# Optimization experiments

Hardware: AMD Instinct MI355X
Metric: run time of the kernel (lower is better)

Reference implementation:

```python
import jax, jax.numpy as jnp
import numpy as np

SLOPE = 25.0   # snntorch surrogate.fast_sigmoid default slope
THR = 1.0      # snntorch Leaky default threshold
BETA = 0.95
SPIKE_STEPS = 4
NUM_HEADS = 16

@jax.custom_vjp
def spike(u):
    # Heaviside forward, fast-sigmoid surrogate backward
    return (u > 0).astype(u.dtype)

def _spike_fwd(u):
    return spike(u), u

def _spike_bwd(u, g):
    return (g / (SLOPE * jnp.abs(u) + 1.0) ** 2,)

spike.defvjp(_spike_fwd, _spike_bwd)

def lif_mean(cur):
    """Run SPIKE_STEPS of a snntorch Leaky neuron (subtract reset, detached)
    with constant input current `cur`; return mean spike train over time."""
    def step(mem, _):
        reset = jax.lax.stop_gradient(spike(mem - THR))
        mem = BETA * mem + cur - reset * THR
        return mem, spike(mem - THR)
    _, spk = jax.lax.scan(step, jnp.zeros_like(cur), None, length=SPIKE_STEPS)
    return spk.mean(axis=0)

def setup_inputs() -> dict:
    B, S, D = 2, 2048, 1024
    key = jax.random.key(0)
    ks = jax.random.split(key, 9)
    std = 1.0 / np.sqrt(D)
    mkw = lambda k: jax.random.uniform(k, (D, D), jnp.float32, -std, std)
    mkb = lambda k: jax.random.uniform(k, (D,), jnp.float32, -std, std)
    return {
        "x": jax.random.normal(ks[0], (B, S, D), jnp.float32),
        "q_w": mkw(ks[1]), "q_b": mkb(ks[2]),
        "k_w": mkw(ks[3]), "k_b": mkb(ks[4]),
        "v_w": mkw(ks[5]), "v_b": mkb(ks[6]),
        "o_w": mkw(ks[7]), "o_b": mkb(ks[8]),
    }

def reference(x, q_w, q_b, k_w, k_b, v_w, v_b, o_w, o_b):
    B, S, D = x.shape
    H = NUM_HEADS
    Hd = D // H
    # projections -> [B, H, S, Hd]  (weights stored [in, out])
    proj = lambda w, b: (x @ w + b).reshape(B, S, H, Hd).transpose(0, 2, 1, 3)
    q, k, v = proj(q_w, q_b), proj(k_w, k_b), proj(v_w, v_b)
    # LIF spiking recurrence, aggregated over time
    q_agg, k_agg, v_agg = lif_mean(q), lif_mean(k), lif_mean(v)
    # standard scaled dot-product attention on aggregated spikes
    scores = jnp.einsum('bhqd,bhkd->bhqk', q_agg, k_agg) / jnp.sqrt(jnp.float32(Hd))
    attn = jax.nn.softmax(scores, axis=-1)
    out = jnp.einsum('bhqk,bhkd->bhqd', attn, v_agg)
    out = out.transpose(0, 2, 1, 3).reshape(B, S, D)
    return out @ o_w + o_b
```

## Files before the change

kernel.cpp:

```cpp
#include <hip/hip_runtime.h>
#include <hip/hip_bf16.h>
#include <stdint.h>

typedef unsigned short u16;
typedef unsigned int u32;
typedef __bf16 bf16x8 __attribute__((ext_vector_type(8)));
typedef float f32x4 __attribute__((ext_vector_type(4)));
typedef float f32x16 __attribute__((ext_vector_type(16)));
typedef u32 u32x4 __attribute__((ext_vector_type(4)));

#define B_   2
#define S_   2048
#define D_   1024
#define H_   16
#define HD_  64

__device__ __forceinline__ u16 f2bf(float f) {
    u32 u = __float_as_uint(f);
    u32 r = (u + 0x7FFFu + ((u >> 16) & 1u)) >> 16;
    return (u16)r;
}
__device__ __forceinline__ float bf2f(u16 s) { return __uint_as_float(((u32)s) << 16); }

__device__ __forceinline__ f32x4 mfma16(bf16x8 a, bf16x8 b, f32x4 c) {
    return __builtin_amdgcn_mfma_f32_16x16x32_bf16(a, b, c, 0, 0, 0);
}
__device__ __forceinline__ f32x16 mfma32(bf16x8 a, bf16x8 b, f32x16 c) {
    return __builtin_amdgcn_mfma_f32_32x32x16_bf16(a, b, c, 0, 0, 0);
}

__device__ __forceinline__ void gl16(const u16* g, u16* l) {
    __builtin_amdgcn_global_load_lds(
        (const __attribute__((address_space(1))) void*)g,
        (__attribute__((address_space(3))) void*)l, 16, 0, 0);
}

__global__ void prep_kernel(const float* __restrict__ x,
                            const float* __restrict__ qw, const float* __restrict__ kw,
                            const float* __restrict__ vw, const float* __restrict__ ow,
                            u16* __restrict__ xbf, u16* __restrict__ wt_all) {
    __shared__ float tile[32][33];
    const int bid = blockIdx.x;
    const int t = threadIdx.x;
    if (bid < 4096) {
        int i = bid * 256 + t;
        float4 v = reinterpret_cast<const float4*>(x)[i];
        uint2 hp;
        hp.x = (u32)f2bf(v.x) | ((u32)f2bf(v.y) << 16);
        hp.y = (u32)f2bf(v.z) | ((u32)f2bf(v.w) << 16);
        reinterpret_cast<uint2*>(xbf)[i] = hp;
        return;
    }
    const int f = bid - 4096;
    const int z = f >> 10;
    const int bi = (f & 1023) >> 5;
    const int bj = f & 31;
    const float* w = (z == 0) ? qw : (z == 1) ? kw : (z == 2) ? vw : ow;
    u16* thi = wt_all + (size_t)z * 1048576;
    const int tx = t & 31, ty = t >> 5;
#pragma unroll
    for (int k = 0; k < 4; k++) {
        int r = ty + k * 8;
        tile[r][tx] = w[(size_t)(bi * 32 + r) * D_ + bj * 32 + tx];
    }
    __syncthreads();
#pragma unroll
    for (int k = 0; k < 4; k++) {
        int r = ty + k * 8;
        thi[(size_t)(bj * 32 + r) * D_ + bi * 32 + tx] = f2bf(tile[tx][r]);
    }
}

__global__ __launch_bounds__(256, 3)
void qkv_gemm(const u16* __restrict__ Ag, const u16* __restrict__ Bg,
              const float* __restrict__ qb, const float* __restrict__ kb,
              const float* __restrict__ vb,
              u16* __restrict__ o0, u16* __restrict__ o1, u16* __restrict__ o2) {
    __shared__ __align__(16) u16 lA[3][128 * 32];
    __shared__ __align__(16) u16 lB[3][128 * 32];

    const int t = threadIdx.x;
    const int flat = blockIdx.y * 24 + blockIdx.x;
    const int swz = (flat & 7) * 96 + (flat >> 3);
    const int m0 = (swz / 24) * 128;
    const int n0 = (swz % 24) * 128;
    const int wid = t >> 6, lane = t & 63;
    const int wm = wid >> 1, wn = wid & 1;
    const int lr = lane & 15, lg = lane >> 4;

    f32x4 acc[4][4] = {};

    auto STAGE = [&](int buf, int kk) {
        const int k0 = kk * 32;
#pragma unroll
        for (int p = 0; p < 2; p++) {
            int idx = p * 256 + wid * 64 + lane;
            int row = idx >> 2, sl = idx & 3;
            int slx = sl ^ ((row >> 1) & 3);
            gl16(Ag + (size_t)(m0 + row) * D_ + k0 + slx * 8,
                 &lA[buf][(p * 256 + wid * 64) * 8]);
            gl16(Bg + (size_t)(n0 + row) * D_ + k0 + slx * 8,
                 &lB[buf][(p * 256 + wid * 64) * 8]);
        }
    };

    STAGE(0, 0);
    STAGE(1, 1);

    for (int kk = 0; kk < 32; ++kk) {
        if (kk < 31) asm volatile("s_waitcnt vmcnt(4)" ::: "memory");
        else         asm volatile("s_waitcnt vmcnt(0)" ::: "memory");
        __builtin_amdgcn_s_barrier();
        if (kk < 30) STAGE((kk + 2) % 3, kk + 2);

        const int cur = kk % 3;
        bf16x8 af[4], bf[4];
#pragma unroll
        for (int m = 0; m < 4; m++) {
            int row = wm * 64 + m * 16 + lr;
            af[m] = *reinterpret_cast<const bf16x8*>(
                &lA[cur][row * 32 + (lg ^ ((row >> 1) & 3)) * 8]);
        }
#pragma unroll
        for (int n = 0; n < 4; n++) {
            int row = wn * 64 + n * 16 + lr;
            bf[n] = *reinterpret_cast<const bf16x8*>(
                &lB[cur][row * 32 + (lg ^ ((row >> 1) & 3)) * 8]);
        }
#pragma unroll
        for (int m = 0; m < 4; m++)
#pragma unroll
            for (int n = 0; n < 4; n++)
                acc[m][n] = mfma16(af[m], bf[n], acc[m][n]);
    }

    const int col0f = n0 + wn * 64;
    const int proj = col0f >> 10;
    const float* bp = (proj == 0) ? qb : (proj == 1) ? kb : vb;
    u16* dst = (proj == 0) ? o0 : (proj == 1) ? o1 : o2;
#pragma unroll
    for (int m = 0; m < 4; m++) {
#pragma unroll
        for (int n = 0; n < 4; n++) {
            u16 agg4[4];
#pragma unroll
            for (int r = 0; r < 4; r++) {
                int row = m0 + wm * 64 + m * 16 + lg * 4 + r;
                int colp = (col0f + n * 16 + lr) & 1023;
                float cur_i = acc[m][n][r] + bp[colp];
                float mem = 0.f;
                int cnt = 0;
#pragma unroll
                for (int tt = 0; tt < 4; tt++) {
                    float reset = (mem > 1.f) ? 1.f : 0.f;
                    mem = 0.95f * mem;
                    mem = mem + cur_i;
                    mem = mem - reset;
                    cnt += (mem > 1.f) ? 1 : 0;
                }
                u16 agg = (u16)(__float_as_uint((float)cnt * 0.25f) >> 16);
                if (proj != 2) {
                    int b = row >> 11, s = row & 2047;
                    int h = colp >> 6, d = colp & 63;
                    dst[((size_t)(b * H_ + h) * S_ + s) * HD_ + d] = agg;
                } else {
                    agg4[r] = agg;
                }
            }
            if (proj == 2) {
                int row0 = m0 + wm * 64 + m * 16 + lg * 4;
                int colp = (col0f + n * 16 + lr) & 1023;
                int b = row0 >> 11, s = row0 & 2047;
                int h = colp >> 6, d = colp & 63;
                uint2 pk;
                pk.x = (u32)agg4[0] | ((u32)agg4[1] << 16);
                pk.y = (u32)agg4[2] | ((u32)agg4[3] << 16);
                *reinterpret_cast<uint2*>(
                    &dst[((size_t)(b * H_ + h) * HD_ + d) * S_ + s]) = pk;
            }
        }
    }
}

__global__ __launch_bounds__(256, 4)
void o_gemm(const u16* __restrict__ Ag, const u16* __restrict__ Bhg,
            const float* __restrict__ bias, float* __restrict__ out) {
    __shared__ __align__(16) u16 lA[3][64 * 32];
    __shared__ __align__(16) u16 lB[3][64 * 32];

    const int t = threadIdx.x;
    const int flat = blockIdx.y * 16 + blockIdx.x;
    const int swz = (flat & 7) * 128 + (flat >> 3);
    const int m0 = (swz >> 4) * 64;
    const int n0 = (swz & 15) * 64;
    const int wid = t >> 6, lane = t & 63;
    const int wm = wid >> 1, wn = wid & 1;
    const int lr = lane & 15, lg = lane >> 4;

    f32x4 acc[2][2] = {};

    auto STAGE = [&](int buf, int kk) {
        const int k0 = kk * 32;
        int idx = wid * 64 + lane;
        int row = idx >> 2, sl = idx & 3;
        int slx = sl ^ ((row >> 1) & 3);
        gl16(Ag + (size_t)(m0 + row) * D_ + k0 + slx * 8,
             &lA[buf][(wid * 64) * 8]);
        gl16(Bhg + (size_t)(n0 + row) * D_ + k0 + slx * 8,
             &lB[buf][(wid * 64) * 8]);
    };

    STAGE(0, 0);
    STAGE(1, 1);

    for (int kk = 0; kk < 32; ++kk) {
        if (kk < 31) asm volatile("s_waitcnt vmcnt(2)" ::: "memory");
        else         asm volatile("s_waitcnt vmcnt(0)" ::: "memory");
        __builtin_amdgcn_s_barrier();
        if (kk < 30) STAGE((kk + 2) % 3, kk + 2);

        const int cur = kk % 3;
        bf16x8 af[2], bf[2];
#pragma unroll
        for (int m = 0; m < 2; m++) {
            int row = wm * 32 + m * 16 + lr;
            af[m] = *reinterpret_cast<const bf16x8*>(
                &lA[cur][row * 32 + (lg ^ ((row >> 1) & 3)) * 8]);
        }
#pragma unroll
        for (int n = 0; n < 2; n++) {
            int row = wn * 32 + n * 16 + lr;
            bf[n] = *reinterpret_cast<const bf16x8*>(
                &lB[cur][row * 32 + (lg ^ ((row >> 1) & 3)) * 8]);
        }
#pragma unroll
        for (int m = 0; m < 2; m++)
#pragma unroll
            for (int n = 0; n < 2; n++)
                acc[m][n] = mfma16(af[m], bf[n], acc[m][n]);
    }

#pragma unroll
    for (int m = 0; m < 2; m++)
#pragma unroll
        for (int n = 0; n < 2; n++)
#pragma unroll
            for (int r = 0; r < 4; r++) {
                int row = m0 + wm * 32 + m * 16 + lg * 4 + r;
                int col = n0 + wn * 32 + n * 16 + lr;
                out[(size_t)row * D_ + col] = acc[m][n][r] + bias[col];
            }
}

__global__ __launch_bounds__(256, 2)
void attn_kernel(const u16* __restrict__ qa, const u16* __restrict__ ka,
                 const u16* __restrict__ vt, u16* __restrict__ oag) {
    __shared__ __align__(16) u16 Kb[2][2][64 * 64];
    __shared__ __align__(16) u16 Vb[2][2][64 * 64];

    const int t = threadIdx.x;
    const int wid = t >> 6, lane = t & 63;
    const int l31 = lane & 31, hi = lane >> 5;
    const int sx = l31 & 7;

    const int flat = blockIdx.y * 16 + blockIdx.x;
    const int swz = (flat & 7) * 64 + (flat >> 3);
    const int bh = swz >> 4;
    const int q0 = (swz & 15) * 128;

    const u16* qbase = qa + (size_t)bh * S_ * HD_;
    const u16* kbase = ka + (size_t)bh * S_ * HD_;
    const u16* vbase = vt + (size_t)bh * HD_ * S_;

    bf16x8 qf[4];
#pragma unroll
    for (int kc = 0; kc < 4; kc++)
        qf[kc] = *reinterpret_cast<const bf16x8*>(
            qbase + (size_t)(q0 + wid * 32 + l31) * HD_ + kc * 16 + hi * 8);

    bf16x8 ones;
#pragma unroll
    for (int j = 0; j < 8; j++) ones[j] = (__bf16)1.0f;

    f32x16 oacc0 = {}, oacc1 = {}, ssum = {};

    auto STAGE = [&](int buf, int kt2) {
#pragma unroll
        for (int s = 0; s < 2; s++) {
#pragma unroll
            for (int p = 0; p < 2; p++) {
                int slot = p * 256 + wid * 64 + lane;
                int row = slot >> 3, sl = slot & 7;
                int slx = sl ^ (row & 7);
                gl16(kbase + (size_t)((kt2 + s) * 64 + row) * HD_ + slx * 8,
                     &Kb[buf][s][(p * 256 + wid * 64) * 8]);
                gl16(vbase + (size_t)row * S_ + (kt2 + s) * 64 + slx * 8,
                     &Vb[buf][s][(p * 256 + wid * 64) * 8]);
            }
        }
    };

    auto COMPUTE = [&](const u16* Kt, const u16* Vt) {
        f32x16 sacc[2] = {};
        __builtin_amdgcn_s_setprio(1);
#pragma unroll
        for (int kc = 0; kc < 4; kc++) {
            int sl = (2 * kc + hi) ^ sx;
            bf16x8 k0 = *reinterpret_cast<const bf16x8*>(&Kt[l31 * 64 + sl * 8]);
            bf16x8 k1 = *reinterpret_cast<const bf16x8*>(&Kt[(32 + l31) * 64 + sl * 8]);
            sacc[0] = mfma32(k0, qf[kc], sacc[0]);
            sacc[1] = mfma32(k1, qf[kc], sacc[1]);
        }
        __builtin_amdgcn_s_setprio(0);
        bf16x8 pa[4];
#pragma unroll
        for (int bb = 0; bb < 2; bb++) {
#pragma unroll
            for (int half = 0; half < 2; half++) {
                float pv[8];
#pragma unroll
                for (int r = 0; r < 8; r++) {
                    float tt = __builtin_fmaf(sacc[bb][half * 8 + r],
                                              0.18033688f, -5.7707802f);
                    asm("v_exp_f32 %0, %1" : "=v"(pv[r]) : "v"(tt));
                }
                u32 A1, A2, B1, B2;
                asm("v_cvt_pk_bf16_f32 %0, %1, %2"
                    : "=v"(A1) : "v"(pv[0]), "v"(pv[1]));
                asm("v_cvt_pk_bf16_f32 %0, %1, %2"
                    : "=v"(A2) : "v"(pv[2]), "v"(pv[3]));
                asm("v_cvt_pk_bf16_f32 %0, %1, %2"
                    : "=v"(B1) : "v"(pv[4]), "v"(pv[5]));
                asm("v_cvt_pk_bf16_f32 %0, %1, %2"
                    : "=v"(B2) : "v"(pv[6]), "v"(pv[7]));
                asm("v_permlane32_swap_b32 %0, %1" : "+v"(A1), "+v"(B1));
                asm("v_permlane32_swap_b32 %0, %1" : "+v"(A2), "+v"(B2));
                u32x4 pw;
                pw.x = A1; pw.y = A2; pw.z = B1; pw.w = B2;
                pa[bb * 2 + half] = __builtin_bit_cast(bf16x8, pw);
            }
        }
        __builtin_amdgcn_s_setprio(1);
#pragma unroll
        for (int k4 = 0; k4 < 4; k4++)
            ssum = mfma32(pa[k4], ones, ssum);
#pragma unroll
        for (int k4 = 0; k4 < 4; k4++) {
            int sl = (2 * k4 + hi) ^ sx;
            bf16x8 v0 = *reinterpret_cast<const bf16x8*>(&Vt[l31 * 64 + sl * 8]);
            bf16x8 v1 = *reinterpret_cast<const bf16x8*>(&Vt[(32 + l31) * 64 + sl * 8]);
            oacc0 = mfma32(pa[k4], v0, oacc0);
            oacc1 = mfma32(pa[k4], v1, oacc1);
        }
        __builtin_amdgcn_s_setprio(0);
    };

    STAGE(0, 0);
    __syncthreads();
    int cur = 0;

    for (int pt = 0; pt < 16; ++pt) {
        if (pt < 15) STAGE(cur ^ 1, (pt + 1) * 2);
        COMPUTE(&Kb[cur][0][0], &Vb[cur][0][0]);
        COMPUTE(&Kb[cur][1][0], &Vb[cur][1][0]);
        __syncthreads();
        cur ^= 1;
    }

    const int b = bh >> 4, h = bh & 15;
#pragma unroll
    for (int r = 0; r < 16; r++) {
        int q = q0 + wid * 32 + (r & 3) + 8 * (r >> 2) + 4 * hi;
        size_t base = (size_t)(b * S_ + q) * D_ + h * 64;
        float v0 = oacc0[r] / ssum[r];
        float v1 = oacc1[r] / ssum[r];
        oag[base + l31] = f2bf(v0);
        oag[base + 32 + l31] = f2bf(v1);
    }
}

extern "C" void kernel_launch(void* const* d_in, const int* in_sizes, int n_in,
                              void* d_out, int out_size, void* d_ws, size_t ws_size,
                              hipStream_t stream) {
    (void)in_sizes; (void)n_in; (void)out_size; (void)ws_size;
    const float* x  = (const float*)d_in[0];
    const float* qw = (const float*)d_in[1];
    const float* qb = (const float*)d_in[2];
    const float* kw = (const float*)d_in[3];
    const float* kb = (const float*)d_in[4];
    const float* vw = (const float*)d_in[5];
    const float* vb = (const float*)d_in[6];
    const float* ow = (const float*)d_in[7];
    const float* ob = (const float*)d_in[8];

    u16* ws = (u16*)d_ws;
    const size_t C = 4194304;
    u16* xbf = ws + 0 * C;
    u16* wt  = ws + 1 * C;
    u16* qag = ws + 2 * C;
    u16* kag = ws + 3 * C;
    u16* vtg = ws + 4 * C;
    u16* oag = ws + 5 * C;

    prep_kernel<<<8192, 256, 0, stream>>>(x, qw, kw, vw, ow, xbf, wt);

    qkv_gemm<<<dim3(24, 32), 256, 0, stream>>>(
        xbf, wt, qb, kb, vb, qag, kag, vtg);
    attn_kernel<<<dim3(16, 32), 256, 0, stream>>>(qag, kag, vtg, oag);
    o_gemm<<<dim3(16, 64), 256, 0, stream>>>(
        oag, wt + 3 * 1048576, ob, (float*)d_out);
}
```

Before: 109.4 us.

## Split attention key tiles across two wave groups with LDS reduction

Doubles the attention block to 512 threads. The two groups of four waves each process one of the two 64-key sub-tiles per iteration for the same 128 queries, and each thread now issues one staging load per sub-tile instead of two. At the end, group 0 writes its partial output and row-sum accumulators to shared memory and group 1 adds them in before normalizing and storing. This is meant to raise wave-level parallelism and latency hiding. The cost is an extra reduction through shared memory, more register pressure under the 512-thread launch bound, and duplicated Q fragment loads.

```diff
diff --git a/kernel.cpp b/kernel.cpp
--- a/kernel.cpp
+++ b/kernel.cpp
@@ -252,7 +252,7 @@
             }
 }
 
-__global__ __launch_bounds__(256, 2)
+__global__ __launch_bounds__(512, 2)
 void attn_kernel(const u16* __restrict__ qa, const u16* __restrict__ ka,
                  const u16* __restrict__ vt, u16* __restrict__ oag) {
     __shared__ __align__(16) u16 Kb[2][2][64 * 64];
@@ -260,6 +260,8 @@
 
     const int t = threadIdx.x;
     const int wid = t >> 6, lane = t & 63;
+    const int grp = wid >> 2;
+    const int qg = wid & 3;
     const int l31 = lane & 31, hi = lane >> 5;
     const int sx = l31 & 7;
 
@@ -276,7 +278,7 @@
 #pragma unroll
     for (int kc = 0; kc < 4; kc++)
         qf[kc] = *reinterpret_cast<const bf16x8*>(
-            qbase + (size_t)(q0 + wid * 32 + l31) * HD_ + kc * 16 + hi * 8);
+            qbase + (size_t)(q0 + qg * 32 + l31) * HD_ + kc * 16 + hi * 8);
 
     bf16x8 ones;
 #pragma unroll
@@ -285,18 +287,15 @@
     f32x16 oacc0 = {}, oacc1 = {}, ssum = {};
 
     auto STAGE = [&](int buf, int kt2) {
+        const int row = t >> 3, sl = t & 7;
+        const int slx = sl ^ (row & 7);
+        const int lbase = (wid * 64) * 8;
 #pragma unroll
         for (int s = 0; s < 2; s++) {
-#pragma unroll
-            for (int p = 0; p < 2; p++) {
-                int slot = p * 256 + wid * 64 + lane;
-                int row = slot >> 3, sl = slot & 7;
-                int slx = sl ^ (row & 7);
-                gl16(kbase + (size_t)((kt2 + s) * 64 + row) * HD_ + slx * 8,
-                     &Kb[buf][s][(p * 256 + wid * 64) * 8]);
-                gl16(vbase + (size_t)row * S_ + (kt2 + s) * 64 + slx * 8,
-                     &Vb[buf][s][(p * 256 + wid * 64) * 8]);
-            }
+            gl16(kbase + (size_t)((kt2 + s) * 64 + row) * HD_ + slx * 8,
+                 &Kb[buf][s][lbase]);
+            gl16(vbase + (size_t)row * S_ + (kt2 + s) * 64 + slx * 8,
+                 &Vb[buf][s][lbase]);
         }
     };
 
@@ -361,21 +360,35 @@
 
     for (int pt = 0; pt < 16; ++pt) {
         if (pt < 15) STAGE(cur ^ 1, (pt + 1) * 2);
-        COMPUTE(&Kb[cur][0][0], &Vb[cur][0][0]);
-        COMPUTE(&Kb[cur][1][0], &Vb[cur][1][0]);
+        COMPUTE(&Kb[cur][grp][0], &Vb[cur][grp][0]);
         __syncthreads();
         cur ^= 1;
     }
 
-    const int b = bh >> 4, h = bh & 15;
-#pragma unroll
-    for (int r = 0; r < 16; r++) {
-        int q = q0 + wid * 32 + (r & 3) + 8 * (r >> 2) + 4 * hi;
-        size_t base = (size_t)(b * S_ + q) * D_ + h * 64;
-        float v0 = oacc0[r] / ssum[r];
-        float v1 = oacc1[r] / ssum[r];
-        oag[base + l31] = f2bf(v0);
-        oag[base + 32 + l31] = f2bf(v1);
+    float* kf = reinterpret_cast<float*>(&Kb[0][0][0]);
+    float* vf = reinterpret_cast<float*>(&Vb[0][0][0]);
+    const int slot = qg * 64 + lane;
+    if (grp == 0) {
+#pragma unroll
+        for (int j = 0; j < 16; j++) {
+            kf[slot + 256 * j] = oacc0[j];
+            kf[slot + 256 * (16 + j)] = ssum[j];
+            vf[slot + 256 * j] = oacc1[j];
+        }
+    }
+    __syncthreads();
+    if (grp == 1) {
+        const int b = bh >> 4, h = bh & 15;
+#pragma unroll
+        for (int r = 0; r < 16; r++) {
+            float o0 = oacc0[r] + kf[slot + 256 * r];
+            float o1 = oacc1[r] + vf[slot + 256 * r];
+            float sd = ssum[r] + kf[slot + 256 * (16 + r)];
+            int q = q0 + qg * 32 + (r & 3) + 8 * (r >> 2) + 4 * hi;
+            size_t base = (size_t)(b * S_ + q) * D_ + h * 64;
+            oag[base + l31] = f2bf(o0 / sd);
+            oag[base + 32 + l31] = f2bf(o1 / sd);
+        }
     }
 }
 
@@ -406,7 +419,7 @@
 
     qkv_gemm<<<dim3(24, 32), 256, 0, stream>>>(
         xbf, wt, qb, kb, vb, qag, kag, vtg);
-    attn_kernel<<<dim3(16, 32), 256, 0, stream>>>(qag, kag, vtg, oag);
+    attn_kernel<<<dim3(16, 32), 512, 0, stream>>>(qag, kag, vtg, oag);
     o_gemm<<<dim3(16, 64), 256, 0, stream>>>(
         oag, wt + 3 * 1048576, ob, (float*)d_out);
 }
```

After: 121.2 us. 1.11x slower.
